# Performance work log

Hardware: AMD Instinct MI355X
Metric: run time of the kernel (lower is better)

## Reference

```python
import jax, jax.numpy as jnp
import numpy as np

B, N, F_IN, F_OUT = 16, 1024, 128, 128

def setup_inputs() -> dict:
    key = jax.random.key(0)
    k1, k2, k3 = jax.random.split(key, 3)
    X = jax.random.normal(k1, (B, N, F_IN), dtype=jnp.float32)
    A = jax.random.uniform(k2, (B, N, N), dtype=jnp.float32)
    W = jax.random.normal(k3, (F_IN, F_OUT), dtype=jnp.float32)
    return {"X": X, "A": A, "W": W}

def reference(X, A, W):
    # A_hat = A + I  (batched add of identity)
    n = A.shape[-1]
    A_hat = A + jnp.eye(n, dtype=A.dtype)  # [B,N,N]
    # D_hat^{-1/2} applied as elementwise row/col scaling (torch builds diag
    # matrices and inverts; mathematically identical for diagonal D).
    deg = jnp.sum(A_hat, axis=-1)               # [B,N]
    d_inv_sqrt = 1.0 / jnp.sqrt(deg)            # [B,N]
    A_norm = A_hat * d_inv_sqrt[:, :, None] * d_inv_sqrt[:, None, :]  # [B,N,N]
    out = jnp.einsum('bnm,bmf->bnf', A_norm, X)  # aggregation bmm
    out = jnp.einsum('bnf,fg->bng', out, W)      # weight matmul
    return out
```

## Files before the change

### kernel.cpp

```cpp
#include <hip/hip_runtime.h>

#define NN 1024
#define FF 128

typedef __attribute__((ext_vector_type(8))) short bf16x8;
typedef __attribute__((ext_vector_type(4))) float f32x4;

__device__ __forceinline__ unsigned short f2bf(float x) {
  unsigned u = __float_as_uint(x);
  u += 0x7fff + ((u >> 16) & 1);
  return (unsigned short)(u >> 16);
}
__device__ __forceinline__ float bf2f(unsigned short b) {
  return __uint_as_float(((unsigned)b) << 16);
}
__device__ __forceinline__ bf16x8 cvt8(float4 a, float4 b) {
  bf16x8 r;
  r[0] = (short)f2bf(a.x); r[1] = (short)f2bf(a.y);
  r[2] = (short)f2bf(a.z); r[3] = (short)f2bf(a.w);
  r[4] = (short)f2bf(b.x); r[5] = (short)f2bf(b.y);
  r[6] = (short)f2bf(b.z); r[7] = (short)f2bf(b.w);
  return r;
}

__device__ __forceinline__ void gl_lds16(const void* g, void* l) {
  __builtin_amdgcn_global_load_lds(
      (const __attribute__((address_space(1))) unsigned*)g,
      (__attribute__((address_space(3))) unsigned*)l, 16, 0, 0);
}

__global__ __launch_bounds__(256) void k_degxw(const float* __restrict__ A,
                                               const float* __restrict__ X,
                                               const float* __restrict__ W,
                                               float* __restrict__ d,
                                               unsigned short* __restrict__ Yt) {
  if (blockIdx.x >= 256) {
    int row  = (blockIdx.x - 256) * 4 + (threadIdx.x >> 6);
    int lane = threadIdx.x & 63;
    const float4* Ar = (const float4*)(A + (size_t)row * NN);
    float s = 0.f;
#pragma unroll
    for (int i = 0; i < 4; ++i) {
      float4 v = Ar[lane + i * 64];
      s += (v.x + v.y) + (v.z + v.w);
    }
#pragma unroll
    for (int off = 32; off > 0; off >>= 1) s += __shfl_down(s, off, 64);
    if (lane == 0) d[row] = rsqrtf(s + 1.0f);
    return;
  }

  __shared__ __align__(16) unsigned short Xs[64 * 128];
  __shared__ __align__(16) unsigned short Ws[128 * 128];
  int t  = threadIdx.x;
  int b  = blockIdx.x >> 4;
  int m0 = (blockIdx.x & 15) * 64;

#pragma unroll
  for (int j = 0; j < 4; ++j) {
    int id = t + j * 256;
    int r = id >> 4, p = id & 15, c = p ^ (r & 15);
    const float* gp = X + ((size_t)(b * NN + m0 + r) * FF + c * 8);
    float4 v0 = *(const float4*)gp;
    float4 v1 = *(const float4*)(gp + 4);
    *(bf16x8*)&Xs[r * 128 + p * 8] = cvt8(v0, v1);
  }
  {
    int f = t >> 1, gh = (t & 1) * 64;
    const float* wrow = W + (size_t)f * FF + gh;
    int c8 = (f >> 3);
    int e  = f & 7;
#pragma unroll
    for (int j4 = 0; j4 < 16; ++j4) {
      float4 wv = *(const float4*)(wrow + j4 * 4);
#pragma unroll
      for (int k = 0; k < 4; ++k) {
        int g = gh + j4 * 4 + k;
        float v = (k == 0) ? wv.x : (k == 1) ? wv.y : (k == 2) ? wv.z : wv.w;
        Ws[g * 128 + ((c8 ^ (g & 15)) * 8) + e] = f2bf(v);
      }
    }
  }
  __syncthreads();

  int wave = t >> 6, lane = t & 63, quad = lane >> 4, l16 = lane & 15;
  f32x4 acc[8];
#pragma unroll
  for (int ct = 0; ct < 8; ++ct) acc[ct] = (f32x4){0.f, 0.f, 0.f, 0.f};

#pragma unroll
  for (int ks = 0; ks < 4; ++ks) {
    int q = ks * 4 + quad;
    bf16x8 a = *(const bf16x8*)&Xs[(wave * 16 + l16) * 128 + (q ^ l16) * 8];
#pragma unroll
    for (int ct = 0; ct < 8; ++ct) {
      bf16x8 w = *(const bf16x8*)&Ws[(ct * 16 + l16) * 128 + (q ^ l16) * 8];
      acc[ct] = __builtin_amdgcn_mfma_f32_16x16x32_bf16(a, w, acc[ct], 0, 0, 0);
    }
  }

  int mb = wave * 16 + quad * 4;
#pragma unroll
  for (int ct = 0; ct < 8; ++ct) {
    int g = ct * 16 + l16;
    ushort4 p;
    p.x = f2bf(acc[ct][0]);
    p.y = f2bf(acc[ct][1]);
    p.z = f2bf(acc[ct][2]);
    p.w = f2bf(acc[ct][3]);
    *(ushort4*)(Yt + (size_t)(b * 128 + g) * NN + m0 + mb) = p;
  }
}

__global__ __launch_bounds__(256, 3) void k_agg(const float* __restrict__ A,
                                                const unsigned short* __restrict__ Yt,
                                                const float* __restrict__ d,
                                                float* __restrict__ out) {
  __shared__ __align__(16) float          Asf[2][32 * 64];
  __shared__ __align__(16) unsigned short Ys[2][128 * 64];
  __shared__ __align__(16) float          dl[NN];
  int t   = threadIdx.x;
  int bid = blockIdx.x;
  int xcd = bid & 7;
  int j   = bid >> 3;
  int b   = xcd + 8 * (j >> 5);
  int n0  = (j & 31) * 32;
  int wave = t >> 6, lane = t & 63, quad = lane >> 4, l16 = lane & 15;
  int wr = wave >> 1, wc = wave & 1;

  const float*          Ab = A  + (size_t)(b * NN + n0) * NN;
  const unsigned short* Yb = Yt + (size_t)b * 128 * NN;

  *(float4*)&dl[t * 4] = *(const float4*)(d + (size_t)b * NN + t * 4);
  __syncthreads();

  int ra = lane >> 4, pa_s = lane & 15;
  int ry_s = lane >> 3, py_s = lane & 7;

  auto issue = [&](int k0, int bufi) {
#pragma unroll
    for (int jj = 0; jj < 2; ++jj) {
      int r = wave * 8 + jj * 4 + ra;
      int c = pa_s ^ (2 * (r & 7));
      gl_lds16(Ab + ((size_t)r * NN + k0 + c * 4),
               &Asf[bufi][(wave * 8 + jj * 4) * 64]);
    }
#pragma unroll
    for (int jj = 0; jj < 4; ++jj) {
      int ry = wave * 32 + jj * 8 + ry_s;
      int c  = py_s ^ (ry & 7);
      gl_lds16(Yb + ((size_t)ry * NN + k0 + c * 8),
               &Ys[bufi][(wave * 32 + jj * 8) * 64]);
    }
  };

  f32x4 acc[4];
#pragma unroll
  for (int ct = 0; ct < 4; ++ct) acc[ct] = (f32x4){0.f, 0.f, 0.f, 0.f};

  int swA = 2 * (l16 & 7);
  issue(0, 0);

#pragma unroll
  for (int s = 0; s < 16; ++s) {
    if (s < 15) {
      issue((s + 1) * 64, (s + 1) & 1);
      asm volatile("s_waitcnt vmcnt(6)" ::: "memory");
    } else {
      asm volatile("s_waitcnt vmcnt(0)" ::: "memory");
    }
    __builtin_amdgcn_s_barrier();
    const float*          as = &Asf[s & 1][0];
    const unsigned short* ys = &Ys[s & 1][0];
    int k0 = s * 64;
    __builtin_amdgcn_s_setprio(1);
#pragma unroll
    for (int ks = 0; ks < 2; ++ks) {
      int cq = ks * 4 + quad;
      int pa = (2 * cq) ^ swA;
      float4 a0 = *(const float4*)&as[(wr * 16 + l16) * 64 + pa * 4];
      float4 a1 = *(const float4*)&as[(wr * 16 + l16) * 64 + pa * 4 + 4];
      float4 dv0 = *(const float4*)&dl[k0 + cq * 8];
      float4 dv1 = *(const float4*)&dl[k0 + cq * 8 + 4];
      a0.x *= dv0.x; a0.y *= dv0.y; a0.z *= dv0.z; a0.w *= dv0.w;
      a1.x *= dv1.x; a1.y *= dv1.y; a1.z *= dv1.z; a1.w *= dv1.w;
      bf16x8 a = cvt8(a0, a1);
#pragma unroll
      for (int ct = 0; ct < 4; ++ct) {
        int cp = (cq ^ (l16 & 7)) * 8;
        bf16x8 y = *(const bf16x8*)&ys[(wc * 64 + ct * 16 + l16) * 64 + cp];
        acc[ct] = __builtin_amdgcn_mfma_f32_16x16x32_bf16(a, y, acc[ct], 0, 0, 0);
      }
    }
    __builtin_amdgcn_s_setprio(0);
    __builtin_amdgcn_sched_barrier(0);
    __builtin_amdgcn_s_barrier();
  }

  int nb = n0 + wr * 16 + quad * 4;
  float4 d4 = *(const float4*)&dl[nb];
#pragma unroll
  for (int ct = 0; ct < 4; ++ct) {
    int g = wc * 64 + ct * 16 + l16;
    ushort4 yv = *(const ushort4*)(Yt + (size_t)(b * 128 + g) * NN + nb);
    float* op = out + ((size_t)(b * NN + nb) * FF + g);
    op[0 * FF] = d4.x * (acc[ct][0] + d4.x * bf2f(yv.x));
    op[1 * FF] = d4.y * (acc[ct][1] + d4.y * bf2f(yv.y));
    op[2 * FF] = d4.z * (acc[ct][2] + d4.z * bf2f(yv.z));
    op[3 * FF] = d4.w * (acc[ct][3] + d4.w * bf2f(yv.w));
  }
}

extern "C" void kernel_launch(void* const* d_in, const int* in_sizes, int n_in,
                              void* d_out, int out_size, void* d_ws, size_t ws_size,
                              hipStream_t stream) {
  const float* X = (const float*)d_in[0];
  const float* A = (const float*)d_in[1];
  const float* W = (const float*)d_in[2];
  float* out = (float*)d_out;

  char* ws = (char*)d_ws;
  float*          dinv = (float*)ws;
  unsigned short* Yt   = (unsigned short*)(ws + 65536);

  k_degxw<<<dim3(256 + 4096), dim3(256), 0, stream>>>(A, X, W, dinv, Yt);
  k_agg  <<<dim3(512),        dim3(256), 0, stream>>>(A, Yt, dinv, out);
}
```

Before: 121.3 us.

## Precompute bf16 adjacency during degree pass and fold column scaling into XW

The degree pass now also writes a bf16 copy of A. The aggregation kernel then streams half-width A tiles directly into the MFMA without per-element scaling or conversion. The column normalisation by d^-1/2 moves into the XW kernel's epilogue, which removes the LDS d table from aggregation and lets it target higher occupancy. The cost is an extra 32MB bf16 write, a third serialized launch, and no longer overlapping the degree and XW work.

```diff
diff --git a/kernel.cpp b/kernel.cpp
--- a/kernel.cpp
+++ b/kernel.cpp
@@ -29,29 +29,34 @@
       (__attribute__((address_space(3))) unsigned*)l, 16, 0, 0);
 }
 
-__global__ __launch_bounds__(256) void k_degxw(const float* __restrict__ A,
-                                               const float* __restrict__ X,
-                                               const float* __restrict__ W,
+__global__ __launch_bounds__(256) void k_degan(const float* __restrict__ A,
                                                float* __restrict__ d,
-                                               unsigned short* __restrict__ Yt) {
-  if (blockIdx.x >= 256) {
-    int row  = (blockIdx.x - 256) * 4 + (threadIdx.x >> 6);
-    int lane = threadIdx.x & 63;
-    const float4* Ar = (const float4*)(A + (size_t)row * NN);
-    float s = 0.f;
-#pragma unroll
-    for (int i = 0; i < 4; ++i) {
-      float4 v = Ar[lane + i * 64];
-      s += (v.x + v.y) + (v.z + v.w);
-    }
-#pragma unroll
-    for (int off = 32; off > 0; off >>= 1) s += __shfl_down(s, off, 64);
-    if (lane == 0) d[row] = rsqrtf(s + 1.0f);
-    return;
-  }
-
+                                               unsigned short* __restrict__ An) {
+  int row  = blockIdx.x * 4 + (threadIdx.x >> 6);
+  int lane = threadIdx.x & 63;
+  const float4* Ar = (const float4*)(A + (size_t)row * NN);
+  unsigned short* Anr = An + (size_t)row * NN;
+  float s = 0.f;
+#pragma unroll
+  for (int i = 0; i < 4; ++i) {
+    float4 v = Ar[lane + i * 64];
+    s += (v.x + v.y) + (v.z + v.w);
+    ushort4 w;
+    w.x = f2bf(v.x); w.y = f2bf(v.y); w.z = f2bf(v.z); w.w = f2bf(v.w);
+    *(ushort4*)(Anr + (size_t)(lane + i * 64) * 4) = w;
+  }
+#pragma unroll
+  for (int off = 32; off > 0; off >>= 1) s += __shfl_down(s, off, 64);
+  if (lane == 0) d[row] = rsqrtf(s + 1.0f);
+}
+
+__global__ __launch_bounds__(256) void k_xw(const float* __restrict__ X,
+                                            const float* __restrict__ W,
+                                            const float* __restrict__ d,
+                                            unsigned short* __restrict__ Yt) {
   __shared__ __align__(16) unsigned short Xs[64 * 128];
   __shared__ __align__(16) unsigned short Ws[128 * 128];
+  __shared__ float dl[64];
   int t  = threadIdx.x;
   int b  = blockIdx.x >> 4;
   int m0 = (blockIdx.x & 15) * 64;
@@ -81,6 +86,7 @@
       }
     }
   }
+  if (t < 64) dl[t] = d[b * NN + m0 + t];
   __syncthreads();
 
   int wave = t >> 6, lane = t & 63, quad = lane >> 4, l16 = lane & 15;
@@ -100,25 +106,25 @@
   }
 
   int mb = wave * 16 + quad * 4;
+  float4 d4 = *(const float4*)&dl[mb];
 #pragma unroll
   for (int ct = 0; ct < 8; ++ct) {
     int g = ct * 16 + l16;
     ushort4 p;
-    p.x = f2bf(acc[ct][0]);
-    p.y = f2bf(acc[ct][1]);
-    p.z = f2bf(acc[ct][2]);
-    p.w = f2bf(acc[ct][3]);
+    p.x = f2bf(d4.x * acc[ct][0]);
+    p.y = f2bf(d4.y * acc[ct][1]);
+    p.z = f2bf(d4.z * acc[ct][2]);
+    p.w = f2bf(d4.w * acc[ct][3]);
     *(ushort4*)(Yt + (size_t)(b * 128 + g) * NN + m0 + mb) = p;
   }
 }
 
-__global__ __launch_bounds__(256, 3) void k_agg(const float* __restrict__ A,
+__global__ __launch_bounds__(256, 4) void k_agg(const unsigned short* __restrict__ An,
                                                 const unsigned short* __restrict__ Yt,
                                                 const float* __restrict__ d,
                                                 float* __restrict__ out) {
-  __shared__ __align__(16) float          Asf[2][32 * 64];
+  __shared__ __align__(16) unsigned short Asb[2][32 * 64];
   __shared__ __align__(16) unsigned short Ys[2][128 * 64];
-  __shared__ __align__(16) float          dl[NN];
   int t   = threadIdx.x;
   int bid = blockIdx.x;
   int xcd = bid & 7;
@@ -128,27 +134,22 @@
   int wave = t >> 6, lane = t & 63, quad = lane >> 4, l16 = lane & 15;
   int wr = wave >> 1, wc = wave & 1;
 
-  const float*          Ab = A  + (size_t)(b * NN + n0) * NN;
+  const unsigned short* Ab = An + (size_t)(b * NN + n0) * NN;
   const unsigned short* Yb = Yt + (size_t)b * 128 * NN;
 
-  *(float4*)&dl[t * 4] = *(const float4*)(d + (size_t)b * NN + t * 4);
-  __syncthreads();
-
-  int ra = lane >> 4, pa_s = lane & 15;
-  int ry_s = lane >> 3, py_s = lane & 7;
+  int rs = lane >> 3, ps = lane & 7;
 
   auto issue = [&](int k0, int bufi) {
-#pragma unroll
-    for (int jj = 0; jj < 2; ++jj) {
-      int r = wave * 8 + jj * 4 + ra;
-      int c = pa_s ^ (2 * (r & 7));
-      gl_lds16(Ab + ((size_t)r * NN + k0 + c * 4),
-               &Asf[bufi][(wave * 8 + jj * 4) * 64]);
+    {
+      int r = wave * 8 + rs;
+      int c = ps ^ (rs & 7);
+      gl_lds16(Ab + ((size_t)r * NN + k0 + c * 8),
+               &Asb[bufi][wave * 8 * 64]);
     }
 #pragma unroll
     for (int jj = 0; jj < 4; ++jj) {
-      int ry = wave * 32 + jj * 8 + ry_s;
-      int c  = py_s ^ (ry & 7);
+      int ry = wave * 32 + jj * 8 + rs;
+      int c  = ps ^ (rs & 7);
       gl_lds16(Yb + ((size_t)ry * NN + k0 + c * 8),
                &Ys[bufi][(wave * 32 + jj * 8) * 64]);
     }
@@ -158,36 +159,27 @@
 #pragma unroll
   for (int ct = 0; ct < 4; ++ct) acc[ct] = (f32x4){0.f, 0.f, 0.f, 0.f};
 
-  int swA = 2 * (l16 & 7);
   issue(0, 0);
 
 #pragma unroll
   for (int s = 0; s < 16; ++s) {
     if (s < 15) {
       issue((s + 1) * 64, (s + 1) & 1);
-      asm volatile("s_waitcnt vmcnt(6)" ::: "memory");
+      asm volatile("s_waitcnt vmcnt(5)" ::: "memory");
     } else {
       asm volatile("s_waitcnt vmcnt(0)" ::: "memory");
     }
     __builtin_amdgcn_s_barrier();
-    const float*          as = &Asf[s & 1][0];
+    const unsigned short* as = &Asb[s & 1][0];
     const unsigned short* ys = &Ys[s & 1][0];
-    int k0 = s * 64;
     __builtin_amdgcn_s_setprio(1);
 #pragma unroll
     for (int ks = 0; ks < 2; ++ks) {
       int cq = ks * 4 + quad;
-      int pa = (2 * cq) ^ swA;
-      float4 a0 = *(const float4*)&as[(wr * 16 + l16) * 64 + pa * 4];
-      float4 a1 = *(const float4*)&as[(wr * 16 + l16) * 64 + pa * 4 + 4];
-      float4 dv0 = *(const float4*)&dl[k0 + cq * 8];
-      float4 dv1 = *(const float4*)&dl[k0 + cq * 8 + 4];
-      a0.x *= dv0.x; a0.y *= dv0.y; a0.z *= dv0.z; a0.w *= dv0.w;
-      a1.x *= dv1.x; a1.y *= dv1.y; a1.z *= dv1.z; a1.w *= dv1.w;
-      bf16x8 a = cvt8(a0, a1);
+      int cp = (cq ^ (l16 & 7)) * 8;
+      bf16x8 a = *(const bf16x8*)&as[(wr * 16 + l16) * 64 + cp];
 #pragma unroll
       for (int ct = 0; ct < 4; ++ct) {
-        int cp = (cq ^ (l16 & 7)) * 8;
         bf16x8 y = *(const bf16x8*)&ys[(wc * 64 + ct * 16 + l16) * 64 + cp];
         acc[ct] = __builtin_amdgcn_mfma_f32_16x16x32_bf16(a, y, acc[ct], 0, 0, 0);
       }
@@ -198,16 +190,16 @@
   }
 
   int nb = n0 + wr * 16 + quad * 4;
-  float4 d4 = *(const float4*)&dl[nb];
+  float4 d4 = *(const float4*)(d + (size_t)b * NN + nb);
 #pragma unroll
   for (int ct = 0; ct < 4; ++ct) {
     int g = wc * 64 + ct * 16 + l16;
     ushort4 yv = *(const ushort4*)(Yt + (size_t)(b * 128 + g) * NN + nb);
     float* op = out + ((size_t)(b * NN + nb) * FF + g);
-    op[0 * FF] = d4.x * (acc[ct][0] + d4.x * bf2f(yv.x));
-    op[1 * FF] = d4.y * (acc[ct][1] + d4.y * bf2f(yv.y));
-    op[2 * FF] = d4.z * (acc[ct][2] + d4.z * bf2f(yv.z));
-    op[3 * FF] = d4.w * (acc[ct][3] + d4.w * bf2f(yv.w));
+    op[0 * FF] = d4.x * (acc[ct][0] + bf2f(yv.x));
+    op[1 * FF] = d4.y * (acc[ct][1] + bf2f(yv.y));
+    op[2 * FF] = d4.z * (acc[ct][2] + bf2f(yv.z));
+    op[3 * FF] = d4.w * (acc[ct][3] + bf2f(yv.w));
   }
 }
 
@@ -222,7 +214,9 @@
   char* ws = (char*)d_ws;
   float*          dinv = (float*)ws;
   unsigned short* Yt   = (unsigned short*)(ws + 65536);
-
-  k_degxw<<<dim3(256 + 4096), dim3(256), 0, stream>>>(A, X, W, dinv, Yt);
-  k_agg  <<<dim3(512),        dim3(256), 0, stream>>>(A, Yt, dinv, out);
-}
+  unsigned short* An   = (unsigned short*)(ws + 65536 + 4194304);
+
+  k_degan<<<dim3(4096), dim3(256), 0, stream>>>(A, dinv, An);
+  k_xw   <<<dim3(256),  dim3(256), 0, stream>>>(X, W, dinv, Yt);
+  k_agg  <<<dim3(512),  dim3(256), 0, stream>>>(An, Yt, dinv, out);
+}
```

After: 124.7 us. 1.03x slower.
